# Kernel optimization log

Hardware: AMD Instinct MI355X
Metric: run time of the kernel (lower is better)

The kernel has to match this reference:

```python
import math
import jax, jax.numpy as jnp
import numpy as np

B, N, D = 16384, 16, 2
HIDDEN, DL = 64, 5
OMEGA = 1.0
CUSP_GAMMA = 1.0 / (D - 1)  # dim=2 -> 1.0


def _linear_params(key, fan_in, fan_out):
    kw, kb = jax.random.split(key)
    bound = 1.0 / math.sqrt(fan_in)
    w = jax.random.uniform(kw, (fan_out, fan_in), jnp.float32, -bound, bound)
    b = jax.random.uniform(kb, (fan_out,), jnp.float32, -bound, bound)
    return w, b


def setup_inputs() -> dict:
    key = jax.random.key(0)
    ks = jax.random.split(key, 9)
    x = jax.random.normal(ks[0], (B, N, D), jnp.float32)
    phi_w0, phi_b0 = _linear_params(ks[1], D + 1, HIDDEN)
    phi_w1, phi_b1 = _linear_params(ks[2], HIDDEN, HIDDEN)
    phi_w2, phi_b2 = _linear_params(ks[3], HIDDEN, DL)
    psi_w0, psi_b0 = _linear_params(ks[4], 6, HIDDEN)
    psi_w1, psi_b1 = _linear_params(ks[5], HIDDEN, HIDDEN)
    psi_w2, psi_b2 = _linear_params(ks[6], HIDDEN, DL)
    rho_w0, rho_b0 = _linear_params(ks[7], 2 * DL, HIDDEN)
    # rho output layer: weight std=0.01 normal, bias zeros (matches torch init)
    rho_w1 = 0.01 * jax.random.normal(ks[8], (1, HIDDEN), jnp.float32)
    rho_b1 = jnp.zeros((1,), jnp.float32)
    return dict(x=x,
                phi_w0=phi_w0, phi_b0=phi_b0, phi_w1=phi_w1, phi_b1=phi_b1,
                phi_w2=phi_w2, phi_b2=phi_b2,
                psi_w0=psi_w0, psi_b0=psi_b0, psi_w1=psi_w1, psi_b1=psi_b1,
                psi_w2=psi_w2, psi_b2=psi_b2,
                rho_w0=rho_w0, rho_b0=rho_b0, rho_w1=rho_w1, rho_b1=rho_b1)


def _mlp3(h, w0, b0, w1, b1, w2, b2):
    h = jax.nn.gelu(h @ w0.T + b0, approximate=False)
    h = jax.nn.gelu(h @ w1.T + b1, approximate=False)
    return h @ w2.T + b2


def reference(x, phi_w0, phi_b0, phi_w1, phi_b1, phi_w2, phi_b2,
              psi_w0, psi_b0, psi_w1, psi_b1, psi_w2, psi_b2,
              rho_w0, rho_b0, rho_w1, rho_b1):
    # one-body branch
    xs = x * math.sqrt(OMEGA)                       # [B,N,D]
    r2 = (xs ** 2).sum(-1, keepdims=True)           # [B,N,1]
    phi_in = jnp.concatenate([xs, r2], -1)          # [B,N,D+1]
    phi_out = _mlp3(phi_in, phi_w0, phi_b0, phi_w1, phi_b1, phi_w2, phi_b2).mean(1)  # [B,dL]

    # two-body branch: vectorized over all N*(N-1)/2 pairs
    ii, jj = jnp.triu_indices(N, k=1)               # static pair index lists, P entries
    dr = x[:, ii, :] - x[:, jj, :]                  # [B,P,D]
    rij = jnp.sqrt((dr ** 2).sum(-1) + 1e-12)       # [B,P]
    feat = jnp.stack([jnp.log1p(rij), rij / (1 + rij), jnp.exp(-rij ** 2),
                      jnp.exp(-0.5 * rij), jnp.exp(-rij), jnp.exp(-2 * rij)], -1)  # [B,P,6]
    psi_out = _mlp3(feat, psi_w0, psi_b0, psi_w1, psi_b1, psi_w2, psi_b2).mean(1)  # [B,dL]
    cusp = CUSP_GAMMA * (rij * jnp.exp(-rij)).sum(-1)  # [B]

    # readout
    rho_in = jnp.concatenate([phi_out, psi_out], -1)   # [B,2*dL]
    h = jax.nn.gelu(rho_in @ rho_w0.T + rho_b0, approximate=False)
    f = (h @ rho_w1.T + rho_b1).squeeze(-1)            # [B]
    return f + cusp
```

## Files before the change

### kernel.cpp

```cpp
#include <hip/hip_runtime.h>
#include <hip/hip_bf16.h>
#include <math.h>

#define B_TOT 16384
#define NPART 16
#define NPAIR 120
#define HID   64
#define DL    5
#define GB    4
#define SROWS 136

typedef __attribute__((ext_vector_type(8))) short short8;
typedef __attribute__((ext_vector_type(4))) float floatx4;

#define CSC      2.45556851f
#define INV_CSC  0.40723744f

__device__ __forceinline__ unsigned pk2(float a, float b) {
    unsigned r;
    asm("v_cvt_pk_bf16_f32 %0, %1, %2" : "=v"(r) : "v"(a), "v"(b));
    return r;
}

__device__ __forceinline__ float gelu_pre(float z) {
    float e = __builtin_amdgcn_exp2f(-z);
    return z * __builtin_amdgcn_rcpf(1.0f + e);
}

__device__ __forceinline__ float gelu_sig(float v) {
    float e = __builtin_amdgcn_exp2f(-2.45556851f * v);
    return v * __builtin_amdgcn_rcpf(1.0f + e);
}

__device__ __forceinline__ float wred(float v) {
    v += __shfl_down(v, 32);
    v += __shfl_down(v, 16);
    v += __shfl_down(v, 8);
    v += __shfl_down(v, 4);
    v += __shfl_down(v, 2);
    v += __shfl_down(v, 1);
    return v;
}

__device__ __forceinline__ int hperm(int ht, int m) {
    return ((ht & 1) << 2) + ((ht >> 1) << 5) + ((m >> 2) << 3) + (m & 3);
}

__global__ __launch_bounds__(256) void jastrow_wave2(
    const float* __restrict__ x,
    const float* __restrict__ phi_w0, const float* __restrict__ phi_b0,
    const float* __restrict__ phi_w1, const float* __restrict__ phi_b1,
    const float* __restrict__ phi_w2, const float* __restrict__ phi_b2,
    const float* __restrict__ psi_w0, const float* __restrict__ psi_b0,
    const float* __restrict__ psi_w1, const float* __restrict__ psi_b1,
    const float* __restrict__ psi_w2, const float* __restrict__ psi_b2,
    const float* __restrict__ rho_w0, const float* __restrict__ rho_b0,
    const float* __restrict__ rho_w1, const float* __restrict__ rho_b1,
    float* __restrict__ out)
{
    const int t    = threadIdx.x;
    const int lane = t & 63;
    const int wv   = t >> 6;
    const int q    = lane >> 4;
    const int m15  = lane & 15;
    const int bg   = blockIdx.x * GB;

    __shared__ __align__(16) unsigned short s_f[GB * SROWS * 8];
    __shared__ float s_cs[GB * 2 * HID];
    unsigned short* sf = s_f + wv * SROWS * 8;

    const float2* x2 = (const float2*)x;
    const int bi = bg + wv;
    float cusp = 0.f;

    {
        {
            int p = lane;
            int u = 119 - p;
            float sq = sqrtf((float)(8 * u + 1));
            int k = (int)((sq - 1.0f) * 0.5f);
            int i = 14 - k;
            int j = p - (i * (31 - i)) / 2 + i + 1;

            float2 xi = x2[bi * NPART + i];
            float2 xj = x2[bi * NPART + j];
            float dx = xi.x - xj.x, dy = xi.y - xj.y;
            float r = sqrtf(dx * dx + dy * dy + 1e-12f);

            float f0 = 0.69314718056f * __builtin_amdgcn_logf(1.f + r);
            float f1 = r * __builtin_amdgcn_rcpf(1.f + r);
            float f3 = __builtin_amdgcn_exp2f(-0.72134752044f * r);
            float f4 = f3 * f3;
            float f5 = f4 * f4;
            float f2 = __builtin_amdgcn_exp2f(-1.44269504089f * r * r);
            cusp += r * f4;

            union { short8 s; unsigned u4[4]; } v;
            v.u4[0] = pk2(f0, f1);
            v.u4[1] = pk2(f2, f3);
            v.u4[2] = pk2(f4, f5);
            v.u4[3] = pk2(1.0f, 0.f);
            *(short8*)&sf[p * 8] = v.s;
        }
        if (lane < NPAIR - 64) {
            int p = 64 + lane;
            int u = 119 - p;
            float sq = sqrtf((float)(8 * u + 1));
            int k = (int)((sq - 1.0f) * 0.5f);
            int i = 14 - k;
            int j = p - (i * (31 - i)) / 2 + i + 1;

            float2 xi = x2[bi * NPART + i];
            float2 xj = x2[bi * NPART + j];
            float dx = xi.x - xj.x, dy = xi.y - xj.y;
            float r = sqrtf(dx * dx + dy * dy + 1e-12f);

            float f0 = 0.69314718056f * __builtin_amdgcn_logf(1.f + r);
            float f1 = r * __builtin_amdgcn_rcpf(1.f + r);
            float f3 = __builtin_amdgcn_exp2f(-0.72134752044f * r);
            float f4 = f3 * f3;
            float f5 = f4 * f4;
            float f2 = __builtin_amdgcn_exp2f(-1.44269504089f * r * r);
            cusp += r * f4;

            union { short8 s; unsigned u4[4]; } v;
            v.u4[0] = pk2(f0, f1);
            v.u4[1] = pk2(f2, f3);
            v.u4[2] = pk2(f4, f5);
            v.u4[3] = pk2(1.0f, 0.f);
            *(short8*)&sf[p * 8] = v.s;
        }
        if (lane >= 48) {
            int n = lane - 48;
            float2 xv = x2[bi * NPART + n];
            float r2 = xv.x * xv.x + xv.y * xv.y;
            union { short8 s; unsigned u4[4]; } w;
            w.u4[0] = pk2(xv.x, xv.y);
            w.u4[1] = pk2(r2, 1.0f);
            w.u4[2] = 0u; w.u4[3] = 0u;
            *(short8*)&sf[(120 + n) * 8] = w.s;
        }
    }
    float cusp_b;
    { float cc = wred(cusp); cusp_b = __shfl(cc, 0); }

    const floatx4 zf4 = {0.f, 0.f, 0.f, 0.f};

    short8 A1p[4];
#pragma unroll
    for (int ht = 0; ht < 4; ++ht) {
        short8 f = (short8)0;
        if (q == 0) {
            int h = hperm(ht, m15);
            const float* w = psi_w0 + h * 6;
            union { short8 s; unsigned u4[4]; } bb;
            bb.u4[0] = pk2(CSC * w[0], CSC * w[1]);
            bb.u4[1] = pk2(CSC * w[2], CSC * w[3]);
            bb.u4[2] = pk2(CSC * w[4], CSC * w[5]);
            bb.u4[3] = pk2(CSC * psi_b0[h], 0.f);
            f = bb.s;
        }
        A1p[ht] = f;
    }
    short8 A2p[4][2];
    floatx4 C1p[4];
#pragma unroll
    for (int ht2 = 0; ht2 < 4; ++ht2) {
        int h2 = hperm(ht2, m15);
#pragma unroll
        for (int ks = 0; ks < 2; ++ks) {
            const floatx4* wp = (const floatx4*)(psi_w1 + h2 * HID + ks * 32 + q * 8);
            floatx4 wa = wp[0], wb = wp[1];
            union { short8 s; unsigned u4[4]; } bb;
            bb.u4[0] = pk2(wa[0], wa[1]); bb.u4[1] = pk2(wa[2], wa[3]);
            bb.u4[2] = pk2(wb[0], wb[1]); bb.u4[3] = pk2(wb[2], wb[3]);
            A2p[ht2][ks] = bb.s;
        }
        int cb = ((ht2 & 1) << 2) + ((ht2 >> 1) << 5) + (q << 3);
        floatx4 bv = *(const floatx4*)(psi_b1 + cb);
        C1p[ht2] = bv * CSC;
    }

    float CS[16];
#pragma unroll
    for (int i = 0; i < 16; ++i) CS[i] = 0.f;

#pragma unroll
    for (int Mt = 0; Mt < 8; ++Mt) {
        short8 b = *(const short8*)&sf[(Mt * 16 + m15) * 8];
        floatx4 d0 = __builtin_amdgcn_mfma_f32_16x16x32_bf16(A1p[0], b, zf4, 0, 0, 0);
        floatx4 d1 = __builtin_amdgcn_mfma_f32_16x16x32_bf16(A1p[1], b, zf4, 0, 0, 0);
        union { short8 s; unsigned u4[4]; } Bk0, Bk1;
        Bk0.u4[0] = pk2(gelu_pre(d0[0]), gelu_pre(d0[1]));
        Bk0.u4[1] = pk2(gelu_pre(d0[2]), gelu_pre(d0[3]));
        Bk0.u4[2] = pk2(gelu_pre(d1[0]), gelu_pre(d1[1]));
        Bk0.u4[3] = pk2(gelu_pre(d1[2]), gelu_pre(d1[3]));
        floatx4 d2 = __builtin_amdgcn_mfma_f32_16x16x32_bf16(A1p[2], b, zf4, 0, 0, 0);
        floatx4 d3 = __builtin_amdgcn_mfma_f32_16x16x32_bf16(A1p[3], b, zf4, 0, 0, 0);
        Bk1.u4[0] = pk2(gelu_pre(d2[0]), gelu_pre(d2[1]));
        Bk1.u4[1] = pk2(gelu_pre(d2[2]), gelu_pre(d2[3]));
        Bk1.u4[2] = pk2(gelu_pre(d3[0]), gelu_pre(d3[1]));
        Bk1.u4[3] = pk2(gelu_pre(d3[2]), gelu_pre(d3[3]));

#pragma unroll
        for (int ht2 = 0; ht2 < 4; ++ht2) {
            floatx4 acc = __builtin_amdgcn_mfma_f32_16x16x32_bf16(A2p[ht2][0], Bk0.s, C1p[ht2], 0, 0, 0);
            acc = __builtin_amdgcn_mfma_f32_16x16x32_bf16(A2p[ht2][1], Bk1.s, acc, 0, 0, 0);
#pragma unroll
            for (int rg = 0; rg < 4; ++rg) {
                float z = acc[rg];
                float rr = __builtin_amdgcn_rcpf(1.0f + __builtin_amdgcn_exp2f(-z));
                if (Mt == 7) {
                    float p = z * rr;
                    p = (m15 < 8) ? p : 0.f;
                    CS[ht2 * 4 + rg] += p;
                } else {
                    CS[ht2 * 4 + rg] = __builtin_fmaf(z, rr, CS[ht2 * 4 + rg]);
                }
            }
        }
    }

#pragma unroll
    for (int i = 0; i < 16; ++i) {
        CS[i] += __shfl_xor(CS[i], 1);
        CS[i] += __shfl_xor(CS[i], 2);
        CS[i] += __shfl_xor(CS[i], 4);
        CS[i] += __shfl_xor(CS[i], 8);
    }
#pragma unroll
    for (int i = 0; i < 16; ++i) {
        if (m15 == i) {
            int h2 = ((i >> 2) & 1) * 4 + (i >> 3) * 32 + q * 8 + (i & 3);
            s_cs[(wv * 2 + 0) * HID + h2] = CS[i];
        }
    }

    __builtin_amdgcn_sched_barrier(0);

    {
        short8 A1f[4];
#pragma unroll
        for (int ht = 0; ht < 4; ++ht) {
            short8 f = (short8)0;
            if (q == 0) {
                int h = hperm(ht, m15);
                const float* w = phi_w0 + h * 3;
                union { short8 s; unsigned u4[4]; } bb;
                bb.u4[0] = pk2(CSC * w[0], CSC * w[1]);
                bb.u4[1] = pk2(CSC * w[2], CSC * phi_b0[h]);
                bb.u4[2] = 0u; bb.u4[3] = 0u;
                f = bb.s;
            }
            A1f[ht] = f;
        }
        short8 A2f[4][2];
        floatx4 C1f[4];
#pragma unroll
        for (int ht2 = 0; ht2 < 4; ++ht2) {
            int h2 = hperm(ht2, m15);
#pragma unroll
            for (int ks = 0; ks < 2; ++ks) {
                const floatx4* wp = (const floatx4*)(phi_w1 + h2 * HID + ks * 32 + q * 8);
                floatx4 wa = wp[0], wb = wp[1];
                union { short8 s; unsigned u4[4]; } bb;
                bb.u4[0] = pk2(wa[0], wa[1]); bb.u4[1] = pk2(wa[2], wa[3]);
                bb.u4[2] = pk2(wb[0], wb[1]); bb.u4[3] = pk2(wb[2], wb[3]);
                A2f[ht2][ks] = bb.s;
            }
            int cb = ((ht2 & 1) << 2) + ((ht2 >> 1) << 5) + (q << 3);
            floatx4 bv = *(const floatx4*)(phi_b1 + cb);
            C1f[ht2] = bv * CSC;
        }

        float CF[16];
        short8 b = *(const short8*)&sf[(120 + m15) * 8];
        floatx4 d0 = __builtin_amdgcn_mfma_f32_16x16x32_bf16(A1f[0], b, zf4, 0, 0, 0);
        floatx4 d1 = __builtin_amdgcn_mfma_f32_16x16x32_bf16(A1f[1], b, zf4, 0, 0, 0);
        union { short8 s; unsigned u4[4]; } Bk0, Bk1;
        Bk0.u4[0] = pk2(gelu_pre(d0[0]), gelu_pre(d0[1]));
        Bk0.u4[1] = pk2(gelu_pre(d0[2]), gelu_pre(d0[3]));
        Bk0.u4[2] = pk2(gelu_pre(d1[0]), gelu_pre(d1[1]));
        Bk0.u4[3] = pk2(gelu_pre(d1[2]), gelu_pre(d1[3]));
        floatx4 d2 = __builtin_amdgcn_mfma_f32_16x16x32_bf16(A1f[2], b, zf4, 0, 0, 0);
        floatx4 d3 = __builtin_amdgcn_mfma_f32_16x16x32_bf16(A1f[3], b, zf4, 0, 0, 0);
        Bk1.u4[0] = pk2(gelu_pre(d2[0]), gelu_pre(d2[1]));
        Bk1.u4[1] = pk2(gelu_pre(d2[2]), gelu_pre(d2[3]));
        Bk1.u4[2] = pk2(gelu_pre(d3[0]), gelu_pre(d3[1]));
        Bk1.u4[3] = pk2(gelu_pre(d3[2]), gelu_pre(d3[3]));

#pragma unroll
        for (int ht2 = 0; ht2 < 4; ++ht2) {
            floatx4 acc = __builtin_amdgcn_mfma_f32_16x16x32_bf16(A2f[ht2][0], Bk0.s, C1f[ht2], 0, 0, 0);
            acc = __builtin_amdgcn_mfma_f32_16x16x32_bf16(A2f[ht2][1], Bk1.s, acc, 0, 0, 0);
#pragma unroll
            for (int rg = 0; rg < 4; ++rg) {
                float z = acc[rg];
                float rr = __builtin_amdgcn_rcpf(1.0f + __builtin_amdgcn_exp2f(-z));
                CF[ht2 * 4 + rg] = z * rr;
            }
        }
#pragma unroll
        for (int i = 0; i < 16; ++i) {
            CF[i] += __shfl_xor(CF[i], 1);
            CF[i] += __shfl_xor(CF[i], 2);
            CF[i] += __shfl_xor(CF[i], 4);
            CF[i] += __shfl_xor(CF[i], 8);
        }
#pragma unroll
        for (int i = 0; i < 16; ++i) {
            if (m15 == i) {
                int h2 = ((i >> 2) & 1) * 4 + (i >> 3) * 32 + q * 8 + (i & 3);
                s_cs[(wv * 2 + 1) * HID + h2] = CF[i];
            }
        }
    }

    {
        const int c = lane;
        float colP = s_cs[(wv * 2 + 0) * HID + c] * INV_CSC;
        float colF = s_cs[(wv * 2 + 1) * HID + c] * INV_CSC;

        float psiv[DL], phiv[DL];
#pragma unroll
        for (int d = 0; d < DL; ++d) {
            float sP = wred(colP * psi_w2[d * HID + c]);
            psiv[d] = __shfl(sP, 0) * (1.0f / NPAIR) + psi_b2[d];
            float sF = wred(colF * phi_w2[d * HID + c]);
            phiv[d] = __shfl(sF, 0) * (1.0f / NPART) + phi_b2[d];
        }

        int j = lane;
        float a = rho_b0[j];
        const float* wr = rho_w0 + j * (2 * DL);
#pragma unroll
        for (int d = 0; d < DL; ++d)
            a += phiv[d] * wr[d] + psiv[d] * wr[DL + d];
        float cv = gelu_sig(a) * rho_w1[j];
        cv = wred(cv);
        if (j == 0) out[bi] = cv + rho_b1[0] + cusp_b;
    }
}

extern "C" void kernel_launch(void* const* d_in, const int* in_sizes, int n_in,
                              void* d_out, int out_size, void* d_ws, size_t ws_size,
                              hipStream_t stream) {
    const float* x      = (const float*)d_in[0];
    const float* phi_w0 = (const float*)d_in[1];
    const float* phi_b0 = (const float*)d_in[2];
    const float* phi_w1 = (const float*)d_in[3];
    const float* phi_b1 = (const float*)d_in[4];
    const float* phi_w2 = (const float*)d_in[5];
    const float* phi_b2 = (const float*)d_in[6];
    const float* psi_w0 = (const float*)d_in[7];
    const float* psi_b0 = (const float*)d_in[8];
    const float* psi_w1 = (const float*)d_in[9];
    const float* psi_b1 = (const float*)d_in[10];
    const float* psi_w2 = (const float*)d_in[11];
    const float* psi_b2 = (const float*)d_in[12];
    const float* rho_w0 = (const float*)d_in[13];
    const float* rho_b0 = (const float*)d_in[14];
    const float* rho_w1 = (const float*)d_in[15];
    const float* rho_b1 = (const float*)d_in[16];

    jastrow_wave2<<<B_TOT / GB, 256, 0, stream>>>(
        x,
        phi_w0, phi_b0, phi_w1, phi_b1, phi_w2, phi_b2,
        psi_w0, psi_b0, psi_w1, psi_b1, psi_w2, psi_b2,
        rho_w0, rho_b0, rho_w1, rho_b1,
        (float*)d_out);
}
```

Baseline: 191.4 us.

## Split each batch element across two waves and swap MFMA operand roles

Each batch element is now handled by two waves instead of one. The waves split the pair tiles and the phi output column groups, and their partial column sums and cusp sums are combined through shared memory after __syncthreads. The second-layer MFMAs swap operands so the activations are the A operand and the weights are B, which lets each lane accumulate per-column sums without the xor-shuffle reductions. This shortens the per-wave serial chain and adds parallelism, at the cost of block-wide barriers, extra shared-memory traffic and duplicated weight packing per wave.

```diff
diff --git a/kernel.cpp b/kernel.cpp
--- a/kernel.cpp
+++ b/kernel.cpp
@@ -7,7 +7,7 @@
 #define NPAIR 120
 #define HID   64
 #define DL    5
-#define GB    4
+#define GB    2
 #define SROWS 136
 
 typedef __attribute__((ext_vector_type(8))) short short8;
@@ -46,7 +46,7 @@
     return ((ht & 1) << 2) + ((ht >> 1) << 5) + ((m >> 2) << 3) + (m & 3);
 }
 
-__global__ __launch_bounds__(256) void jastrow_wave2(
+__global__ __launch_bounds__(256) void jastrow_fused(
     const float* __restrict__ x,
     const float* __restrict__ phi_w0, const float* __restrict__ phi_b0,
     const float* __restrict__ phi_w1, const float* __restrict__ phi_b1,
@@ -58,50 +58,53 @@
     const float* __restrict__ rho_w1, const float* __restrict__ rho_b1,
     float* __restrict__ out)
 {
-    const int t    = threadIdx.x;
-    const int lane = t & 63;
-    const int wv   = t >> 6;
-    const int q    = lane >> 4;
-    const int m15  = lane & 15;
-    const int bg   = blockIdx.x * GB;
+    const int t     = threadIdx.x;
+    const int lane  = t & 63;
+    const int wv    = t >> 6;
+    const int q     = lane >> 4;
+    const int m15   = lane & 15;
+    const int h     = wv & 1;
+    const int bslot = wv >> 1;
+    const int bg    = blockIdx.x * GB;
+    const int bi    = bg + bslot;
 
     __shared__ __align__(16) unsigned short s_f[GB * SROWS * 8];
-    __shared__ float s_cs[GB * 2 * HID];
-    unsigned short* sf = s_f + wv * SROWS * 8;
-
+    __shared__ float s_csP[GB * 2 * 4 * 4 * 16];
+    __shared__ float s_csF[GB * 4 * 4 * 16];
+    __shared__ float s_cusp[GB * 2];
+
+    unsigned short* sf = s_f + bslot * SROWS * 8;
     const float2* x2 = (const float2*)x;
-    const int bi = bg + wv;
     float cusp = 0.f;
 
-    {
-        {
-            int p = lane;
-            int u = 119 - p;
-            float sq = sqrtf((float)(8 * u + 1));
-            int k = (int)((sq - 1.0f) * 0.5f);
-            int i = 14 - k;
-            int j = p - (i * (31 - i)) / 2 + i + 1;
-
-            float2 xi = x2[bi * NPART + i];
-            float2 xj = x2[bi * NPART + j];
-            float dx = xi.x - xj.x, dy = xi.y - xj.y;
-            float r = sqrtf(dx * dx + dy * dy + 1e-12f);
-
-            float f0 = 0.69314718056f * __builtin_amdgcn_logf(1.f + r);
-            float f1 = r * __builtin_amdgcn_rcpf(1.f + r);
-            float f3 = __builtin_amdgcn_exp2f(-0.72134752044f * r);
-            float f4 = f3 * f3;
-            float f5 = f4 * f4;
-            float f2 = __builtin_amdgcn_exp2f(-1.44269504089f * r * r);
-            cusp += r * f4;
-
-            union { short8 s; unsigned u4[4]; } v;
-            v.u4[0] = pk2(f0, f1);
-            v.u4[1] = pk2(f2, f3);
-            v.u4[2] = pk2(f4, f5);
-            v.u4[3] = pk2(1.0f, 0.f);
-            *(short8*)&sf[p * 8] = v.s;
-        }
+    if (h == 0) {
+        int p = lane;
+        int u = 119 - p;
+        float sq = sqrtf((float)(8 * u + 1));
+        int k = (int)((sq - 1.0f) * 0.5f);
+        int i = 14 - k;
+        int j = p - (i * (31 - i)) / 2 + i + 1;
+
+        float2 xi = x2[bi * NPART + i];
+        float2 xj = x2[bi * NPART + j];
+        float dx = xi.x - xj.x, dy = xi.y - xj.y;
+        float r = sqrtf(dx * dx + dy * dy + 1e-12f);
+
+        float f0 = 0.69314718056f * __builtin_amdgcn_logf(1.f + r);
+        float f1 = r * __builtin_amdgcn_rcpf(1.f + r);
+        float f3 = __builtin_amdgcn_exp2f(-0.72134752044f * r);
+        float f4 = f3 * f3;
+        float f5 = f4 * f4;
+        float f2 = __builtin_amdgcn_exp2f(-1.44269504089f * r * r);
+        cusp = r * f4;
+
+        union { short8 s; unsigned u4[4]; } v;
+        v.u4[0] = pk2(f0, f1);
+        v.u4[1] = pk2(f2, f3);
+        v.u4[2] = pk2(f4, f5);
+        v.u4[3] = pk2(1.0f, 0.f);
+        *(short8*)&sf[p * 8] = v.s;
+    } else {
         if (lane < NPAIR - 64) {
             int p = 64 + lane;
             int u = 119 - p;
@@ -121,7 +124,7 @@
             float f4 = f3 * f3;
             float f5 = f4 * f4;
             float f2 = __builtin_amdgcn_exp2f(-1.44269504089f * r * r);
-            cusp += r * f4;
+            cusp = r * f4;
 
             union { short8 s; unsigned u4[4]; } v;
             v.u4[0] = pk2(f0, f1);
@@ -141,102 +144,13 @@
             *(short8*)&sf[(120 + n) * 8] = w.s;
         }
     }
-    float cusp_b;
-    { float cc = wred(cusp); cusp_b = __shfl(cc, 0); }
+    {
+        float cc = wred(cusp);
+        if (lane == 0) s_cusp[bslot * 2 + h] = cc;
+    }
+    __syncthreads();
 
     const floatx4 zf4 = {0.f, 0.f, 0.f, 0.f};
-
-    short8 A1p[4];
-#pragma unroll
-    for (int ht = 0; ht < 4; ++ht) {
-        short8 f = (short8)0;
-        if (q == 0) {
-            int h = hperm(ht, m15);
-            const float* w = psi_w0 + h * 6;
-            union { short8 s; unsigned u4[4]; } bb;
-            bb.u4[0] = pk2(CSC * w[0], CSC * w[1]);
-            bb.u4[1] = pk2(CSC * w[2], CSC * w[3]);
-            bb.u4[2] = pk2(CSC * w[4], CSC * w[5]);
-            bb.u4[3] = pk2(CSC * psi_b0[h], 0.f);
-            f = bb.s;
-        }
-        A1p[ht] = f;
-    }
-    short8 A2p[4][2];
-    floatx4 C1p[4];
-#pragma unroll
-    for (int ht2 = 0; ht2 < 4; ++ht2) {
-        int h2 = hperm(ht2, m15);
-#pragma unroll
-        for (int ks = 0; ks < 2; ++ks) {
-            const floatx4* wp = (const floatx4*)(psi_w1 + h2 * HID + ks * 32 + q * 8);
-            floatx4 wa = wp[0], wb = wp[1];
-            union { short8 s; unsigned u4[4]; } bb;
-            bb.u4[0] = pk2(wa[0], wa[1]); bb.u4[1] = pk2(wa[2], wa[3]);
-            bb.u4[2] = pk2(wb[0], wb[1]); bb.u4[3] = pk2(wb[2], wb[3]);
-            A2p[ht2][ks] = bb.s;
-        }
-        int cb = ((ht2 & 1) << 2) + ((ht2 >> 1) << 5) + (q << 3);
-        floatx4 bv = *(const floatx4*)(psi_b1 + cb);
-        C1p[ht2] = bv * CSC;
-    }
-
-    float CS[16];
-#pragma unroll
-    for (int i = 0; i < 16; ++i) CS[i] = 0.f;
-
-#pragma unroll
-    for (int Mt = 0; Mt < 8; ++Mt) {
-        short8 b = *(const short8*)&sf[(Mt * 16 + m15) * 8];
-        floatx4 d0 = __builtin_amdgcn_mfma_f32_16x16x32_bf16(A1p[0], b, zf4, 0, 0, 0);
-        floatx4 d1 = __builtin_amdgcn_mfma_f32_16x16x32_bf16(A1p[1], b, zf4, 0, 0, 0);
-        union { short8 s; unsigned u4[4]; } Bk0, Bk1;
-        Bk0.u4[0] = pk2(gelu_pre(d0[0]), gelu_pre(d0[1]));
-        Bk0.u4[1] = pk2(gelu_pre(d0[2]), gelu_pre(d0[3]));
-        Bk0.u4[2] = pk2(gelu_pre(d1[0]), gelu_pre(d1[1]));
-        Bk0.u4[3] = pk2(gelu_pre(d1[2]), gelu_pre(d1[3]));
-        floatx4 d2 = __builtin_amdgcn_mfma_f32_16x16x32_bf16(A1p[2], b, zf4, 0, 0, 0);
-        floatx4 d3 = __builtin_amdgcn_mfma_f32_16x16x32_bf16(A1p[3], b, zf4, 0, 0, 0);
-        Bk1.u4[0] = pk2(gelu_pre(d2[0]), gelu_pre(d2[1]));
-        Bk1.u4[1] = pk2(gelu_pre(d2[2]), gelu_pre(d2[3]));
-        Bk1.u4[2] = pk2(gelu_pre(d3[0]), gelu_pre(d3[1]));
-        Bk1.u4[3] = pk2(gelu_pre(d3[2]), gelu_pre(d3[3]));
-
-#pragma unroll
-        for (int ht2 = 0; ht2 < 4; ++ht2) {
-            floatx4 acc = __builtin_amdgcn_mfma_f32_16x16x32_bf16(A2p[ht2][0], Bk0.s, C1p[ht2], 0, 0, 0);
-            acc = __builtin_amdgcn_mfma_f32_16x16x32_bf16(A2p[ht2][1], Bk1.s, acc, 0, 0, 0);
-#pragma unroll
-            for (int rg = 0; rg < 4; ++rg) {
-                float z = acc[rg];
-                float rr = __builtin_amdgcn_rcpf(1.0f + __builtin_amdgcn_exp2f(-z));
-                if (Mt == 7) {
-                    float p = z * rr;
-                    p = (m15 < 8) ? p : 0.f;
-                    CS[ht2 * 4 + rg] += p;
-                } else {
-                    CS[ht2 * 4 + rg] = __builtin_fmaf(z, rr, CS[ht2 * 4 + rg]);
-                }
-            }
-        }
-    }
-
-#pragma unroll
-    for (int i = 0; i < 16; ++i) {
-        CS[i] += __shfl_xor(CS[i], 1);
-        CS[i] += __shfl_xor(CS[i], 2);
-        CS[i] += __shfl_xor(CS[i], 4);
-        CS[i] += __shfl_xor(CS[i], 8);
-    }
-#pragma unroll
-    for (int i = 0; i < 16; ++i) {
-        if (m15 == i) {
-            int h2 = ((i >> 2) & 1) * 4 + (i >> 3) * 32 + q * 8 + (i & 3);
-            s_cs[(wv * 2 + 0) * HID + h2] = CS[i];
-        }
-    }
-
-    __builtin_amdgcn_sched_barrier(0);
 
     {
         short8 A1f[4];
@@ -244,82 +158,157 @@
         for (int ht = 0; ht < 4; ++ht) {
             short8 f = (short8)0;
             if (q == 0) {
-                int h = hperm(ht, m15);
-                const float* w = phi_w0 + h * 3;
+                int hr = hperm(ht, m15);
+                const float* w = phi_w0 + hr * 3;
                 union { short8 s; unsigned u4[4]; } bb;
                 bb.u4[0] = pk2(CSC * w[0], CSC * w[1]);
-                bb.u4[1] = pk2(CSC * w[2], CSC * phi_b0[h]);
+                bb.u4[1] = pk2(CSC * w[2], CSC * phi_b0[hr]);
                 bb.u4[2] = 0u; bb.u4[3] = 0u;
                 f = bb.s;
             }
             A1f[ht] = f;
         }
-        short8 A2f[4][2];
-        floatx4 C1f[4];
-#pragma unroll
-        for (int ht2 = 0; ht2 < 4; ++ht2) {
-            int h2 = hperm(ht2, m15);
-#pragma unroll
-            for (int ks = 0; ks < 2; ++ks) {
-                const floatx4* wp = (const floatx4*)(phi_w1 + h2 * HID + ks * 32 + q * 8);
+        short8 B2f[2][2];
+        float b1f[2];
+#pragma unroll
+        for (int cgl = 0; cgl < 2; ++cgl) {
+            const int cg = h * 2 + cgl;
+#pragma unroll
+            for (int Kc = 0; Kc < 2; ++Kc) {
+                const floatx4* wp = (const floatx4*)(phi_w1 + (cg * 16 + m15) * HID + Kc * 32 + q * 8);
                 floatx4 wa = wp[0], wb = wp[1];
                 union { short8 s; unsigned u4[4]; } bb;
                 bb.u4[0] = pk2(wa[0], wa[1]); bb.u4[1] = pk2(wa[2], wa[3]);
                 bb.u4[2] = pk2(wb[0], wb[1]); bb.u4[3] = pk2(wb[2], wb[3]);
-                A2f[ht2][ks] = bb.s;
-            }
-            int cb = ((ht2 & 1) << 2) + ((ht2 >> 1) << 5) + (q << 3);
-            floatx4 bv = *(const floatx4*)(phi_b1 + cb);
-            C1f[ht2] = bv * CSC;
-        }
-
-        float CF[16];
+                B2f[cgl][Kc] = bb.s;
+            }
+            b1f[cgl] = CSC * phi_b1[cg * 16 + m15];
+        }
+
         short8 b = *(const short8*)&sf[(120 + m15) * 8];
         floatx4 d0 = __builtin_amdgcn_mfma_f32_16x16x32_bf16(A1f[0], b, zf4, 0, 0, 0);
         floatx4 d1 = __builtin_amdgcn_mfma_f32_16x16x32_bf16(A1f[1], b, zf4, 0, 0, 0);
-        union { short8 s; unsigned u4[4]; } Bk0, Bk1;
-        Bk0.u4[0] = pk2(gelu_pre(d0[0]), gelu_pre(d0[1]));
-        Bk0.u4[1] = pk2(gelu_pre(d0[2]), gelu_pre(d0[3]));
-        Bk0.u4[2] = pk2(gelu_pre(d1[0]), gelu_pre(d1[1]));
-        Bk0.u4[3] = pk2(gelu_pre(d1[2]), gelu_pre(d1[3]));
+        union { short8 s; unsigned u4[4]; } Ak0, Ak1;
+        Ak0.u4[0] = pk2(gelu_pre(d0[0]), gelu_pre(d0[1]));
+        Ak0.u4[1] = pk2(gelu_pre(d0[2]), gelu_pre(d0[3]));
+        Ak0.u4[2] = pk2(gelu_pre(d1[0]), gelu_pre(d1[1]));
+        Ak0.u4[3] = pk2(gelu_pre(d1[2]), gelu_pre(d1[3]));
         floatx4 d2 = __builtin_amdgcn_mfma_f32_16x16x32_bf16(A1f[2], b, zf4, 0, 0, 0);
         floatx4 d3 = __builtin_amdgcn_mfma_f32_16x16x32_bf16(A1f[3], b, zf4, 0, 0, 0);
-        Bk1.u4[0] = pk2(gelu_pre(d2[0]), gelu_pre(d2[1]));
-        Bk1.u4[1] = pk2(gelu_pre(d2[2]), gelu_pre(d2[3]));
-        Bk1.u4[2] = pk2(gelu_pre(d3[0]), gelu_pre(d3[1]));
-        Bk1.u4[3] = pk2(gelu_pre(d3[2]), gelu_pre(d3[3]));
-
-#pragma unroll
-        for (int ht2 = 0; ht2 < 4; ++ht2) {
-            floatx4 acc = __builtin_amdgcn_mfma_f32_16x16x32_bf16(A2f[ht2][0], Bk0.s, C1f[ht2], 0, 0, 0);
-            acc = __builtin_amdgcn_mfma_f32_16x16x32_bf16(A2f[ht2][1], Bk1.s, acc, 0, 0, 0);
+        Ak1.u4[0] = pk2(gelu_pre(d2[0]), gelu_pre(d2[1]));
+        Ak1.u4[1] = pk2(gelu_pre(d2[2]), gelu_pre(d2[3]));
+        Ak1.u4[2] = pk2(gelu_pre(d3[0]), gelu_pre(d3[1]));
+        Ak1.u4[3] = pk2(gelu_pre(d3[2]), gelu_pre(d3[3]));
+
+#pragma unroll
+        for (int cgl = 0; cgl < 2; ++cgl) {
+            floatx4 C1 = {b1f[cgl], b1f[cgl], b1f[cgl], b1f[cgl]};
+            floatx4 acc = __builtin_amdgcn_mfma_f32_16x16x32_bf16(Ak0.s, B2f[cgl][0], C1, 0, 0, 0);
+            acc = __builtin_amdgcn_mfma_f32_16x16x32_bf16(Ak1.s, B2f[cgl][1], acc, 0, 0, 0);
+            float s = 0.f;
 #pragma unroll
             for (int rg = 0; rg < 4; ++rg) {
                 float z = acc[rg];
                 float rr = __builtin_amdgcn_rcpf(1.0f + __builtin_amdgcn_exp2f(-z));
-                CF[ht2 * 4 + rg] = z * rr;
-            }
-        }
-#pragma unroll
-        for (int i = 0; i < 16; ++i) {
-            CF[i] += __shfl_xor(CF[i], 1);
-            CF[i] += __shfl_xor(CF[i], 2);
-            CF[i] += __shfl_xor(CF[i], 4);
-            CF[i] += __shfl_xor(CF[i], 8);
-        }
-#pragma unroll
-        for (int i = 0; i < 16; ++i) {
-            if (m15 == i) {
-                int h2 = ((i >> 2) & 1) * 4 + (i >> 3) * 32 + q * 8 + (i & 3);
-                s_cs[(wv * 2 + 1) * HID + h2] = CF[i];
-            }
-        }
-    }
+                s = __builtin_fmaf(z, rr, s);
+            }
+            const int cg = h * 2 + cgl;
+            s_csF[((bslot * 4 + cg) * 4 + q) * 16 + m15] = s;
+        }
+    }
+
+    __builtin_amdgcn_sched_barrier(0);
 
     {
-        const int c = lane;
-        float colP = s_cs[(wv * 2 + 0) * HID + c] * INV_CSC;
-        float colF = s_cs[(wv * 2 + 1) * HID + c] * INV_CSC;
+        short8 A1p[4];
+#pragma unroll
+        for (int ht = 0; ht < 4; ++ht) {
+            short8 f = (short8)0;
+            if (q == 0) {
+                int hr = hperm(ht, m15);
+                const float* w = psi_w0 + hr * 6;
+                union { short8 s; unsigned u4[4]; } bb;
+                bb.u4[0] = pk2(CSC * w[0], CSC * w[1]);
+                bb.u4[1] = pk2(CSC * w[2], CSC * w[3]);
+                bb.u4[2] = pk2(CSC * w[4], CSC * w[5]);
+                bb.u4[3] = pk2(CSC * psi_b0[hr], 0.f);
+                f = bb.s;
+            }
+            A1p[ht] = f;
+        }
+        short8 B2p[4][2];
+        float b1s[4];
+#pragma unroll
+        for (int cg = 0; cg < 4; ++cg) {
+#pragma unroll
+            for (int Kc = 0; Kc < 2; ++Kc) {
+                const floatx4* wp = (const floatx4*)(psi_w1 + (cg * 16 + m15) * HID + Kc * 32 + q * 8);
+                floatx4 wa = wp[0], wb = wp[1];
+                union { short8 s; unsigned u4[4]; } bb;
+                bb.u4[0] = pk2(wa[0], wa[1]); bb.u4[1] = pk2(wa[2], wa[3]);
+                bb.u4[2] = pk2(wb[0], wb[1]); bb.u4[3] = pk2(wb[2], wb[3]);
+                B2p[cg][Kc] = bb.s;
+            }
+            b1s[cg] = CSC * psi_b1[cg * 16 + m15];
+        }
+
+        float cs[4] = {0.f, 0.f, 0.f, 0.f};
+#pragma unroll
+        for (int ti = 0; ti < 4; ++ti) {
+            const int Mt = h * 4 + ti;
+            short8 b = *(const short8*)&sf[(Mt * 16 + m15) * 8];
+            floatx4 d0 = __builtin_amdgcn_mfma_f32_16x16x32_bf16(A1p[0], b, zf4, 0, 0, 0);
+            floatx4 d1 = __builtin_amdgcn_mfma_f32_16x16x32_bf16(A1p[1], b, zf4, 0, 0, 0);
+            union { short8 s; unsigned u4[4]; } Ak0, Ak1;
+            Ak0.u4[0] = pk2(gelu_pre(d0[0]), gelu_pre(d0[1]));
+            Ak0.u4[1] = pk2(gelu_pre(d0[2]), gelu_pre(d0[3]));
+            Ak0.u4[2] = pk2(gelu_pre(d1[0]), gelu_pre(d1[1]));
+            Ak0.u4[3] = pk2(gelu_pre(d1[2]), gelu_pre(d1[3]));
+            floatx4 d2 = __builtin_amdgcn_mfma_f32_16x16x32_bf16(A1p[2], b, zf4, 0, 0, 0);
+            floatx4 d3 = __builtin_amdgcn_mfma_f32_16x16x32_bf16(A1p[3], b, zf4, 0, 0, 0);
+            Ak1.u4[0] = pk2(gelu_pre(d2[0]), gelu_pre(d2[1]));
+            Ak1.u4[1] = pk2(gelu_pre(d2[2]), gelu_pre(d2[3]));
+            Ak1.u4[2] = pk2(gelu_pre(d3[0]), gelu_pre(d3[1]));
+            Ak1.u4[3] = pk2(gelu_pre(d3[2]), gelu_pre(d3[3]));
+
+            const bool ghost = (h == 1) && (ti == 3) && (q >= 2);
+#pragma unroll
+            for (int cg = 0; cg < 4; ++cg) {
+                floatx4 C1 = {b1s[cg], b1s[cg], b1s[cg], b1s[cg]};
+                floatx4 acc = __builtin_amdgcn_mfma_f32_16x16x32_bf16(Ak0.s, B2p[cg][0], C1, 0, 0, 0);
+                acc = __builtin_amdgcn_mfma_f32_16x16x32_bf16(Ak1.s, B2p[cg][1], acc, 0, 0, 0);
+                if (!ghost) {
+#pragma unroll
+                    for (int rg = 0; rg < 4; ++rg) {
+                        float z = acc[rg];
+                        float rr = __builtin_amdgcn_rcpf(1.0f + __builtin_amdgcn_exp2f(-z));
+                        cs[cg] = __builtin_fmaf(z, rr, cs[cg]);
+                    }
+                }
+            }
+        }
+#pragma unroll
+        for (int cg = 0; cg < 4; ++cg)
+            s_csP[(((bslot * 2 + h) * 4 + q) * 4 + cg) * 16 + m15] = cs[cg];
+    }
+
+    __syncthreads();
+
+    if (h == 0) {
+        const int br = bslot;
+        const int c  = lane;
+        const int cw = c >> 4, cm = c & 15;
+        float colP = 0.f, colF = 0.f;
+#pragma unroll
+        for (int w2 = 0; w2 < 2; ++w2)
+#pragma unroll
+            for (int qq = 0; qq < 4; ++qq)
+                colP += s_csP[(((br * 2 + w2) * 4 + qq) * 4 + cw) * 16 + cm];
+#pragma unroll
+        for (int qq = 0; qq < 4; ++qq)
+            colF += s_csF[((br * 4 + cw) * 4 + qq) * 16 + cm];
+        colP *= INV_CSC;
+        colF *= INV_CSC;
 
         float psiv[DL], phiv[DL];
 #pragma unroll
@@ -336,9 +325,10 @@
 #pragma unroll
         for (int d = 0; d < DL; ++d)
             a += phiv[d] * wr[d] + psiv[d] * wr[DL + d];
+        float cuspb = s_cusp[br * 2] + s_cusp[br * 2 + 1];
         float cv = gelu_sig(a) * rho_w1[j];
         cv = wred(cv);
-        if (j == 0) out[bi] = cv + rho_b1[0] + cusp_b;
+        if (j == 0) out[bg + br] = cv + rho_b1[0] + cuspb;
     }
 }
 
@@ -363,7 +353,7 @@
     const float* rho_w1 = (const float*)d_in[15];
     const float* rho_b1 = (const float*)d_in[16];
 
-    jastrow_wave2<<<B_TOT / GB, 256, 0, stream>>>(
+    jastrow_fused<<<B_TOT / GB, 256, 0, stream>>>(
         x,
         phi_w0, phi_b0, phi_w1, phi_b1, phi_w2, phi_b2,
         psi_w0, psi_b0, psi_w1, psi_b1, psi_w2, psi_b2,
```

Measured after the change: 254.2 us. +32.8%, slower.
